# Kernel tuning notes

Hardware: AMD Instinct MI355X
Metric: run time of the kernel (lower is better)

The kernel has to match this reference:

```python
import jax, jax.numpy as jnp
import numpy as np

N_A, N_B = 50000, 20000   # authors, teams
E0, E1, E2 = 600000, 300000, 300000  # coauthor(A->A), writes(A->B), influences(B->A)
D = 128                   # in_feats = out_feats


def setup_inputs() -> dict:
    key = jax.random.key(0)
    ks = jax.random.split(key, 12)
    h_A = jax.random.normal(ks[0], (N_A, D), jnp.float32)
    h_B = jax.random.normal(ks[1], (N_B, D), jnp.float32)
    W0 = jax.random.normal(ks[2], (D, D), jnp.float32) * 0.05
    W1 = jax.random.normal(ks[3], (D, D), jnp.float32) * 0.05
    W2 = jax.random.normal(ks[4], (D, D), jnp.float32) * 0.05
    b0 = jnp.zeros((D,), jnp.float32)
    b1 = jnp.zeros((D,), jnp.float32)
    b2 = jnp.zeros((D,), jnp.float32)
    src0 = jax.random.randint(ks[5], (E0,), 0, N_A)
    dst0 = jax.random.randint(ks[6], (E0,), 0, N_A)
    src1 = jax.random.randint(ks[7], (E1,), 0, N_A)
    dst1 = jax.random.randint(ks[8], (E1,), 0, N_B)
    src2 = jax.random.randint(ks[9], (E2,), 0, N_B)
    dst2 = jax.random.randint(ks[10], (E2,), 0, N_A)
    return dict(h_A=h_A, h_B=h_B, W0=W0, b0=b0, W1=W1, b1=b1, W2=W2, b2=b2,
                src0=src0, dst0=dst0, src1=src1, dst1=dst1, src2=src2, dst2=dst2)


def _graph_conv(x_src, W, b, src, dst, n_dst):
    """DGL GraphConv, norm='both': out = D_dst^{-1/2} A D_src^{-1/2} (X W) + b."""
    n_src = x_src.shape[0]
    ones = jnp.ones(src.shape[0], x_src.dtype)
    deg_out = jnp.clip(jax.ops.segment_sum(ones, src, num_segments=n_src), 1.0)
    deg_in = jnp.clip(jax.ops.segment_sum(ones, dst, num_segments=n_dst), 1.0)
    m = (x_src @ W) * (deg_out ** -0.5)[:, None]          # [n_src, D]
    agg = jax.ops.segment_sum(m[src], dst, num_segments=n_dst)  # [n_dst, D]
    return agg * (deg_in ** -0.5)[:, None] + b


def reference(h_A, h_B, W0, b0, W1, b1, W2, b2, src0, dst0, src1, dst1, src2, dst2):
    # HeteroGraphConv(aggregate='sum'): sum per-relation GraphConv outputs per dst ntype.
    out_A = (_graph_conv(h_A, W0, b0, src0, dst0, N_A)
             + _graph_conv(h_B, W2, b2, src2, dst2, N_A))
    out_B = _graph_conv(h_A, W1, b1, src1, dst1, N_B)
    # every ntype present in h receives an output, so no passthrough branch fires
    return out_A, out_B
```

## Files before the change

kernel.cpp:

```cpp
#include <hip/hip_runtime.h>

#define NA 50000
#define NB 20000
#define NE0 600000
#define NE1 300000
#define NE2 300000
#define DD 128
#define SUB 32768
#define PER 18750


typedef short bf16x8 __attribute__((ext_vector_type(8)));
typedef float f32x4 __attribute__((ext_vector_type(4)));

__device__ __forceinline__ unsigned short f2bf(float f) {
    union { float f; unsigned int u; } v; v.f = f;
    unsigned int r = v.u + 0x7fffu + ((v.u >> 16) & 1u);
    return (unsigned short)(r >> 16);
}
__device__ __forceinline__ float lo2f(unsigned int u) {
    union { float f; unsigned int u; } v; v.u = u << 16;
    return v.f;
}
__device__ __forceinline__ float hi2f(unsigned int u) {
    union { float f; unsigned int u; } v; v.u = u & 0xffff0000u;
    return v.f;
}

__global__ __launch_bounds__(1024) void hist_kernel(
    const int* __restrict__ s0, const int* __restrict__ d0,
    const int* __restrict__ s1, const int* __restrict__ d1,
    const int* __restrict__ s2, const int* __restrict__ d2,
    unsigned int* __restrict__ Pd,
    unsigned char* __restrict__ rank0, unsigned char* __restrict__ rank1,
    unsigned char* __restrict__ rank2,
    const float* __restrict__ W0, const float* __restrict__ W1,
    const float* __restrict__ W2, unsigned short* __restrict__ Wt)
{
    __shared__ unsigned int h32[SUB / 2];
    const int cfg = blockIdx.z;
    if (cfg == 6) {
        int flat = blockIdx.y * 2 + blockIdx.x;
        if (flat >= 48) return;
        int i = flat * 1024 + threadIdx.x;
        int w = i >> 14, r = i & (DD * DD - 1);
        int c = r >> 7, k = r & (DD - 1);
        const float* W = (w == 0) ? W0 : ((w == 1) ? W1 : W2);
        Wt[i] = f2bf(W[k * DD + c]);
        return;
    }
    const int En[6] = {NE0, NE0, NE1, NE1, NE2, NE2};
    const int Kn[6] = {NA, NA, NA, NB, NB, NA};
    const int Gn[6] = {32, 32, 16, 16, 16, 16};
    const int Po[6] = {0, 1600000, 3200000, 4000000, 4320000, 4640000};
    int E = En[cfg], K = Kn[cfg], G = Gn[cfg];
    int sub = blockIdx.x, g = blockIdx.y;
    int nsub = (K + SUB - 1) / SUB;
    if (sub >= nsub || g >= G) return;
    const int* keys = cfg == 0 ? s0 : cfg == 1 ? d0 : cfg == 2 ? s1
                    : cfg == 3 ? d1 : cfg == 4 ? s2 : d2;
    unsigned char* rk = cfg == 1 ? rank0 : cfg == 3 ? rank1
                      : cfg == 5 ? rank2 : (unsigned char*)0;
    int lo = sub * SUB;
    int hi = min(K, lo + SUB);
    int cnt = hi - lo;
    for (int i = threadIdx.x; i < SUB / 2; i += 1024) h32[i] = 0;
    __syncthreads();
    int e1 = min(E, g * PER + PER);
    for (int e = g * PER + threadIdx.x; e < e1; e += 1024) {
        int k = keys[e];
        if (k >= lo && k < hi) {
            int kk = k - lo;
            unsigned sh = (kk & 1) << 4;
            unsigned old = atomicAdd(&h32[kk >> 1], 1u << sh);
            if (rk) rk[e] = (unsigned char)((old >> sh) & 0xffu);
        }
    }
    __syncthreads();
    unsigned int* outp = Pd + ((Po[cfg] + g * K + lo) >> 1);
    for (int i = threadIdx.x; i < cnt / 2; i += 1024) outp[i] = h32[i];
}

__global__ __launch_bounds__(256) void reduce2(
    const unsigned short* __restrict__ P16, int* __restrict__ ideg,
    float* __restrict__ rdeg, int* __restrict__ spart,
    unsigned char* __restrict__ cum8)
{
    __shared__ int lds[256];
    const int y = blockIdx.y;
    const int Ro[6] = {0, NA, 2 * NA, 3 * NA, 3 * NA + NB, 3 * NA + 2 * NB};
    const int Kr[6] = {NA, NA, NA, NB, NB, NA};
    const int Gr[6] = {32, 32, 16, 16, 16, 16};
    const int Po[6] = {0, 1600000, 3200000, 4000000, 4320000, 4640000};
    const int Co[6] = {0, 0, 0, 1600000, 0, 1920000};
    int K = Kr[y], G = Gr[y];
    int b = blockIdx.x, t = threadIdx.x;
    int nchunk = (K + 255) >> 8;
    if (b >= nchunk) return;
    int key = b * 256 + t;
    bool valid = key < K;
    bool din = (y == 1) || (y == 3) || (y == 5);
    const unsigned short* p = P16 + Po[y] + key;
    unsigned char* cb = cum8 + Co[y] + key;
    int run = 0;
    for (int g = 0; g < G; ++g) {
        if (din && valid) cb[g * K] = (unsigned char)run;
        run += valid ? p[g * K] : 0;
    }
    if (valid) {
        ideg[Ro[y] + key] = run;
        rdeg[Ro[y] + key] = rsqrtf(fmaxf((float)run, 1.f));
    }
    if (din) {
        int slot = (y - 1) >> 1;
        lds[t] = run; __syncthreads();
        for (int o = 128; o > 0; o >>= 1) {
            if (t < o) lds[t] += lds[t + o];
            __syncthreads();
        }
        if (t == 0) spart[slot * 256 + b] = lds[0];
    }
}

__global__ __launch_bounds__(256) void scan3(
    const int* __restrict__ ideg, const int* __restrict__ spart,
    int* __restrict__ rp)
{
    __shared__ int lds[256];
    const int y = blockIdx.y;
    const int off[3] = {NA, 3 * NA, 3 * NA + 2 * NB};
    const int nn[3]  = {NA, NB, NA};
    const int ro[3]  = {0, NA, NA + NB};
    int n = nn[y];
    int b = blockIdx.x, t = threadIdx.x;
    if (b * 1024 >= n) return;

    lds[t] = (t < 4 * b) ? spart[y * 256 + t] : 0;
    __syncthreads();
    for (int o = 128; o > 0; o >>= 1) {
        if (t < o) lds[t] += lds[t + o];
        __syncthreads();
    }
    int pv = lds[0];
    __syncthreads();

    const int* deg = ideg + off[y];
    int base = b * 1024 + t * 4;
    int v[4]; int tsum = 0;
    #pragma unroll
    for (int k = 0; k < 4; ++k) {
        v[k] = (base + k < n) ? deg[base + k] : 0;
        tsum += v[k];
    }
    lds[t] = tsum; __syncthreads();
    for (int o = 1; o < 256; o <<= 1) {
        int x = (t >= o) ? lds[t - o] : 0;
        __syncthreads();
        lds[t] += x;
        __syncthreads();
    }
    int run = lds[t] - tsum + pv;
    int* rowptr = rp + ro[y];
    #pragma unroll
    for (int k = 0; k < 4; ++k) {
        if (base + k < n) rowptr[base + k] = run;
        run += v[k];
    }
}

__global__ __launch_bounds__(512) void work_kernel(
    const int* __restrict__ s0, const int* __restrict__ d0,
    const int* __restrict__ s1, const int* __restrict__ d1,
    const int* __restrict__ s2, const int* __restrict__ d2,
    const unsigned char* __restrict__ cum8,
    const unsigned char* __restrict__ rank0, const unsigned char* __restrict__ rank1,
    const unsigned char* __restrict__ rank2,
    const int* __restrict__ rp,
    int* __restrict__ csr0, int* __restrict__ csr1, int* __restrict__ csr2,
    const float* __restrict__ hA, const float* __restrict__ hB,
    const unsigned short* __restrict__ Wt, const float* __restrict__ rdeg,
    unsigned short* __restrict__ mA0, unsigned short* __restrict__ mA1,
    unsigned short* __restrict__ mB2)
{
    int bx = blockIdx.x;
    int wid  = threadIdx.x >> 6;
    int lane = threadIdx.x & 63;
    int quad = lane >> 4;
    int l16  = lane & 15;
    if (bx < 391) {
        int base = bx * 128 + wid * 16;
        if (base >= NA) return;
        int arow = base + l16;
        if (arow >= NA) arow = NA - 1;
        bf16x8 a[4];
        #pragma unroll
        for (int kk = 0; kk < 4; ++kk) {
            const float4* p = (const float4*)(hA + (size_t)arow * DD + kk * 32 + quad * 8);
            float4 u = p[0], w = p[1];
            bf16x8 t;
            t[0] = (short)f2bf(u.x); t[1] = (short)f2bf(u.y);
            t[2] = (short)f2bf(u.z); t[3] = (short)f2bf(u.w);
            t[4] = (short)f2bf(w.x); t[5] = (short)f2bf(w.y);
            t[6] = (short)f2bf(w.z); t[7] = (short)f2bf(w.w);
            a[kk] = t;
        }
        float rs0[4], rs1[4]; int orow0 = base + quad * 4;
        #pragma unroll
        for (int r = 0; r < 4; ++r) {
            int orow = orow0 + r; int c = orow < NA ? orow : 0;
            rs0[r] = rdeg[c]; rs1[r] = rdeg[2 * NA + c];
        }
        #pragma unroll
        for (int ct = 0; ct < 8; ++ct) {
            f32x4 acc0 = {0.f, 0.f, 0.f, 0.f};
            f32x4 acc1 = {0.f, 0.f, 0.f, 0.f};
            const unsigned short* wp = Wt + (size_t)(ct * 16 + l16) * DD + quad * 8;
            #pragma unroll
            for (int kk = 0; kk < 4; ++kk) {
                bf16x8 b0 = *(const bf16x8*)(wp + kk * 32);
                bf16x8 b1 = *(const bf16x8*)(wp + 16384 + kk * 32);
                acc0 = __builtin_amdgcn_mfma_f32_16x16x32_bf16(a[kk], b0, acc0, 0, 0, 0);
                acc1 = __builtin_amdgcn_mfma_f32_16x16x32_bf16(a[kk], b1, acc1, 0, 0, 0);
            }
            #pragma unroll
            for (int r = 0; r < 4; ++r) {
                int orow = orow0 + r;
                if (orow < NA) {
                    mA0[(size_t)orow * DD + ct * 16 + l16] = f2bf(acc0[r] * rs0[r]);
                    mA1[(size_t)orow * DD + ct * 16 + l16] = f2bf(acc1[r] * rs1[r]);
                }
            }
        }
        return;
    }
    if (bx < 548) {
        int base = (bx - 391) * 128 + wid * 16;
        if (base >= NB) return;
        int arow = base + l16;
        if (arow >= NB) arow = NB - 1;
        bf16x8 a[4];
        #pragma unroll
        for (int kk = 0; kk < 4; ++kk) {
            const float4* p = (const float4*)(hB + (size_t)arow * DD + kk * 32 + quad * 8);
            float4 u = p[0], w = p[1];
            bf16x8 t;
            t[0] = (short)f2bf(u.x); t[1] = (short)f2bf(u.y);
            t[2] = (short)f2bf(u.z); t[3] = (short)f2bf(u.w);
            t[4] = (short)f2bf(w.x); t[5] = (short)f2bf(w.y);
            t[6] = (short)f2bf(w.z); t[7] = (short)f2bf(w.w);
            a[kk] = t;
        }
        float rs[4]; int orow0 = base + quad * 4;
        #pragma unroll
        for (int r = 0; r < 4; ++r) {
            int orow = orow0 + r;
            rs[r] = rdeg[3 * NA + NB + (orow < NB ? orow : 0)];
        }
        #pragma unroll
        for (int ct = 0; ct < 8; ++ct) {
            f32x4 acc = {0.f, 0.f, 0.f, 0.f};
            const unsigned short* wp = Wt + 32768 + (size_t)(ct * 16 + l16) * DD + quad * 8;
            #pragma unroll
            for (int kk = 0; kk < 4; ++kk) {
                bf16x8 b = *(const bf16x8*)(wp + kk * 32);
                acc = __builtin_amdgcn_mfma_f32_16x16x32_bf16(a[kk], b, acc, 0, 0, 0);
            }
            #pragma unroll
            for (int r = 0; r < 4; ++r) {
                int orow = orow0 + r;
                if (orow < NB)
                    mB2[(size_t)orow * DD + ct * 16 + l16] = f2bf(acc[r] * rs[r]);
            }
        }
        return;
    }
    int pb = bx - 548;
    int z = (pb < 586) ? 0 : (pb < 879) ? 1 : 2;
    const int zb[3] = {0, 586, 879};
    const int En[3] = {NE0, NE1, NE2};
    const int Kn[3] = {NA, NB, NA};
    const int Co[3] = {0, 1600000, 1920000};
    const int ro[3] = {0, NA, NA + NB};
    int E = En[z], K = Kn[z];
    const int* src = z == 0 ? s0 : z == 1 ? s1 : s2;
    const int* dst = z == 0 ? d0 : z == 1 ? d1 : d2;
    const unsigned char* rk = z == 0 ? rank0 : z == 1 ? rank1 : rank2;
    int* csr = z == 0 ? csr0 : z == 1 ? csr1 : csr2;
    int e0 = (pb - zb[z]) * 1024 + threadIdx.x;
    int e1 = e0 + 512;
    bool v0 = e0 < E, v1 = e1 < E;
    int ce0 = v0 ? e0 : 0, ce1 = v1 ? e1 : 0;
    int d_0 = dst[ce0];
    int d_1 = dst[ce1];
    int r_0 = rk[ce0];
    int r_1 = rk[ce1];
    int s_0 = src[ce0];
    int s_1 = src[ce1];
    int g0 = ce0 / PER;
    int g1 = ce1 / PER;
    int p0 = rp[ro[z] + d_0] + (int)cum8[Co[z] + g0 * K + d_0] + r_0;
    int p1 = rp[ro[z] + d_1] + (int)cum8[Co[z] + g1 * K + d_1] + r_1;
    if (v0) csr[p0] = s_0;
    if (v1) csr[p1] = s_1;
}

__device__ __forceinline__ void acc8(float* o, uint4 u) {
    o[0] += lo2f(u.x); o[1] += hi2f(u.x);
    o[2] += lo2f(u.y); o[3] += hi2f(u.y);
    o[4] += lo2f(u.z); o[5] += hi2f(u.z);
    o[6] += lo2f(u.w); o[7] += hi2f(u.w);
}
__device__ __forceinline__ void gather_rel4(
    const char* __restrict__ Mb, const int* __restrict__ csr,
    int st, int n, int lane, int q, unsigned laneoff, float* o)
{
    for (int ch = 0; ch < n; ch += 64) {
        int m = n - ch; if (m > 64) m = 64;
        int idx = csr[st + ch + (lane < m ? lane : m - 1)];
        int j = 0;
        for (; j + 8 <= m; j += 8) {
            int sA = __shfl(idx, j + q);
            int sB = __shfl(idx, j + 4 + q);
            uint4 uA = *(const uint4*)(Mb + (((unsigned)sA << 8) + laneoff));
            uint4 uB = *(const uint4*)(Mb + (((unsigned)sB << 8) + laneoff));
            acc8(o, uA); acc8(o, uB);
        }
        if (j + 4 <= m) {
            int s = __shfl(idx, j + q);
            uint4 u = *(const uint4*)(Mb + (((unsigned)s << 8) + laneoff));
            acc8(o, u);
            j += 4;
        }
        if (j < m) {
            int jj = j + q;
            float w = jj < m ? 1.f : 0.f;
            int s = __shfl(idx, jj < m ? jj : m - 1);
            uint4 u = *(const uint4*)(Mb + (((unsigned)s << 8) + laneoff));
            o[0] = fmaf(w, lo2f(u.x), o[0]); o[1] = fmaf(w, hi2f(u.x), o[1]);
            o[2] = fmaf(w, lo2f(u.y), o[2]); o[3] = fmaf(w, hi2f(u.y), o[3]);
            o[4] = fmaf(w, lo2f(u.z), o[4]); o[5] = fmaf(w, hi2f(u.z), o[5]);
            o[6] = fmaf(w, lo2f(u.w), o[6]); o[7] = fmaf(w, hi2f(u.w), o[7]);
        }
    }
}

__global__ __launch_bounds__(256) void gather_all(
    const unsigned short* __restrict__ mA0, const unsigned short* __restrict__ mA1,
    const unsigned short* __restrict__ mB2,
    const int* __restrict__ csr0, const int* __restrict__ csr1,
    const int* __restrict__ csr2,
    const int* __restrict__ rp, const int* __restrict__ ideg,
    const float* __restrict__ rdeg,
    const float* __restrict__ b0, const float* __restrict__ b1,
    const float* __restrict__ b2,
    float* __restrict__ out)
{
    int wid = threadIdx.x >> 6, lane = threadIdx.x & 63;
    int q = lane >> 4, l16 = lane & 15;
    unsigned laneoff = (unsigned)l16 * 16u;
    float v[8];
    #pragma unroll
    for (int i = 0; i < 8; ++i) v[i] = 0.f;
    float* op;
    const float *bia, *bib;

    if (blockIdx.x < 12500) {
        int d = blockIdx.x * 4 + wid;
        float c[8];
        #pragma unroll
        for (int i = 0; i < 8; ++i) c[i] = 0.f;
        gather_rel4((const char*)mA0, csr0, rp[d], ideg[NA + d], lane, q, laneoff, v);
        gather_rel4((const char*)mB2, csr2, rp[NA + NB + d], ideg[3 * NA + 2 * NB + d],
                    lane, q, laneoff, c);
        float r0 = rdeg[NA + d], r2 = rdeg[3 * NA + 2 * NB + d];
        #pragma unroll
        for (int i = 0; i < 8; ++i) v[i] = v[i] * r0 + c[i] * r2;
        op = out + (size_t)d * DD;
        bia = b0; bib = b2;
    } else {
        int d = (blockIdx.x - 12500) * 4 + wid;
        gather_rel4((const char*)mA1, csr1, rp[NA + d], ideg[3 * NA + d],
                    lane, q, laneoff, v);
        float r1 = rdeg[3 * NA + d];
        #pragma unroll
        for (int i = 0; i < 8; ++i) v[i] *= r1;
        op = out + (size_t)(NA + d) * DD;
        bia = b1; bib = 0;
    }

    #pragma unroll
    for (int i = 0; i < 8; ++i) {
        v[i] += __shfl_down(v[i], 32);
        v[i] += __shfl_down(v[i], 16);
    }
    if (lane < 16) {
        int col = l16 * 8;
        float4 ba0 = *(const float4*)(bia + col);
        float4 ba1 = *(const float4*)(bia + col + 4);
        if (bib) {
            float4 bb0 = *(const float4*)(bib + col);
            float4 bb1 = *(const float4*)(bib + col + 4);
            ba0.x += bb0.x; ba0.y += bb0.y; ba0.z += bb0.z; ba0.w += bb0.w;
            ba1.x += bb1.x; ba1.y += bb1.y; ba1.z += bb1.z; ba1.w += bb1.w;
        }
        float4 o0 = {v[0] + ba0.x, v[1] + ba0.y, v[2] + ba0.z, v[3] + ba0.w};
        float4 o1 = {v[4] + ba1.x, v[5] + ba1.y, v[6] + ba1.z, v[7] + ba1.w};
        *(float4*)(op + col) = o0;
        *(float4*)(op + col + 4) = o1;
    }
}

extern "C" void kernel_launch(void* const* d_in, const int* in_sizes, int n_in,
                              void* d_out, int out_size, void* d_ws, size_t ws_size,
                              hipStream_t stream) {
    const float* hA = (const float*)d_in[0];
    const float* hB = (const float*)d_in[1];
    const float* W0 = (const float*)d_in[2];
    const float* b0 = (const float*)d_in[3];
    const float* W1 = (const float*)d_in[4];
    const float* b1 = (const float*)d_in[5];
    const float* W2 = (const float*)d_in[6];
    const float* b2 = (const float*)d_in[7];
    const int* s0 = (const int*)d_in[8];
    const int* d0 = (const int*)d_in[9];
    const int* s1 = (const int*)d_in[10];
    const int* d1 = (const int*)d_in[11];
    const int* s2 = (const int*)d_in[12];
    const int* d2 = (const int*)d_in[13];
    float* out = (float*)d_out;
    char* ws = (char*)d_ws;

    unsigned short* mA0 = (unsigned short*)(ws + 0);
    unsigned short* mA1 = (unsigned short*)(ws + 12800000);
    unsigned short* mB2 = (unsigned short*)(ws + 25600000);
    unsigned short* P16 = (unsigned short*)(ws + 0);
    unsigned int*   Pd  = (unsigned int*)(ws + 0);
    unsigned short* Wt  = (unsigned short*)(ws + 30720000);
    float* rdeg         = (float*)(ws + 30818304);
    int*   ideg         = (int*)  (ws + 31778304);
    int*   rp           = (int*)  (ws + 32738304);
    int*   spart        = (int*)  (ws + 33218304);
    unsigned char* cum8 = (unsigned char*)(ws + 33221376);
    unsigned char* rank0= (unsigned char*)(ws + 35941376);
    unsigned char* rank1= (unsigned char*)(ws + 36541376);
    unsigned char* rank2= (unsigned char*)(ws + 36841376);
    int*   csr0         = (int*)  (ws + 37141376);
    int*   csr1         = (int*)  (ws + 39541376);
    int*   csr2         = (int*)  (ws + 40741376);

    hist_kernel<<<dim3(2, 32, 7), 1024, 0, stream>>>(s0, d0, s1, d1, s2, d2,
        Pd, rank0, rank1, rank2, W0, W1, W2, Wt);
    reduce2<<<dim3(196, 6), 256, 0, stream>>>(P16, ideg, rdeg, spart, cum8);
    scan3<<<dim3(49, 3), 256, 0, stream>>>(ideg, spart, rp);
    work_kernel<<<548 + 1172, 512, 0, stream>>>(s0, d0, s1, d1, s2, d2,
        cum8, rank0, rank1, rank2, rp, csr0, csr1, csr2,
        hA, hB, Wt, rdeg, mA0, mA1, mB2);
    gather_all<<<12500 + 5000, 256, 0, stream>>>(mA0, mA1, mB2,
        csr0, csr1, csr2, rp, ideg, rdeg, b0, b1, b2, out);
}
```

Measured before the change: 237.3 us.

## Precompute CSR scatter positions in scan and store CSR indices as u16

The scan kernel now also writes a per-(group, destination) absolute position table, rowptr plus cum8, into the output buffer, which serves as scratch. The scatter kernel then does one lookup instead of two, and each thread handles four edges instead of two, launched on half as many blocks. CSR source indices are stored as 16-bit values, which fit because node counts are at most 50000, to cut index bytes in the scatter and gather passes. In exchange the scan kernel does a long serial per-thread loop writing about 2.7M ints with few blocks. That extra scan work could offset the savings.

```diff
diff --git a/kernel.cpp b/kernel.cpp
--- a/kernel.cpp
+++ b/kernel.cpp
@@ -124,13 +124,16 @@
 
 __global__ __launch_bounds__(256) void scan3(
     const int* __restrict__ ideg, const int* __restrict__ spart,
-    int* __restrict__ rp)
+    int* __restrict__ rp, const unsigned char* __restrict__ cum8,
+    int* __restrict__ pos32)
 {
     __shared__ int lds[256];
     const int y = blockIdx.y;
     const int off[3] = {NA, 3 * NA, 3 * NA + 2 * NB};
     const int nn[3]  = {NA, NB, NA};
     const int ro[3]  = {0, NA, NA + NB};
+    const int Gy[3]  = {32, 16, 16};
+    const int Coy[3] = {0, 1600000, 1920000};
     int n = nn[y];
     int b = blockIdx.x, t = threadIdx.x;
     if (b * 1024 >= n) return;
@@ -161,10 +164,24 @@
     }
     int run = lds[t] - tsum + pv;
     int* rowptr = rp + ro[y];
+    int rv[4];
     #pragma unroll
     for (int k = 0; k < 4; ++k) {
+        rv[k] = run;
         if (base + k < n) rowptr[base + k] = run;
         run += v[k];
+    }
+    int G = Gy[y];
+    const int Co_ = Coy[y];
+    for (int g = 0; g < G; ++g) {
+        #pragma unroll
+        for (int k = 0; k < 4; ++k) {
+            int key = base + k;
+            if (key < n) {
+                int c = Co_ + g * n + key;
+                pos32[c] = rv[k] + (int)cum8[c];
+            }
+        }
     }
 }
 
@@ -172,11 +189,11 @@
     const int* __restrict__ s0, const int* __restrict__ d0,
     const int* __restrict__ s1, const int* __restrict__ d1,
     const int* __restrict__ s2, const int* __restrict__ d2,
-    const unsigned char* __restrict__ cum8,
     const unsigned char* __restrict__ rank0, const unsigned char* __restrict__ rank1,
     const unsigned char* __restrict__ rank2,
-    const int* __restrict__ rp,
-    int* __restrict__ csr0, int* __restrict__ csr1, int* __restrict__ csr2,
+    const int* __restrict__ pos32,
+    unsigned short* __restrict__ csr0, unsigned short* __restrict__ csr1,
+    unsigned short* __restrict__ csr2,
     const float* __restrict__ hA, const float* __restrict__ hB,
     const unsigned short* __restrict__ Wt, const float* __restrict__ rdeg,
     unsigned short* __restrict__ mA0, unsigned short* __restrict__ mA1,
@@ -275,33 +292,40 @@
         return;
     }
     int pb = bx - 548;
-    int z = (pb < 586) ? 0 : (pb < 879) ? 1 : 2;
-    const int zb[3] = {0, 586, 879};
+    int z = (pb < 293) ? 0 : (pb < 440) ? 1 : 2;
+    const int zb[3] = {0, 293, 440};
     const int En[3] = {NE0, NE1, NE2};
     const int Kn[3] = {NA, NB, NA};
     const int Co[3] = {0, 1600000, 1920000};
-    const int ro[3] = {0, NA, NA + NB};
     int E = En[z], K = Kn[z];
     const int* src = z == 0 ? s0 : z == 1 ? s1 : s2;
     const int* dst = z == 0 ? d0 : z == 1 ? d1 : d2;
     const unsigned char* rk = z == 0 ? rank0 : z == 1 ? rank1 : rank2;
-    int* csr = z == 0 ? csr0 : z == 1 ? csr1 : csr2;
-    int e0 = (pb - zb[z]) * 1024 + threadIdx.x;
-    int e1 = e0 + 512;
-    bool v0 = e0 < E, v1 = e1 < E;
-    int ce0 = v0 ? e0 : 0, ce1 = v1 ? e1 : 0;
-    int d_0 = dst[ce0];
-    int d_1 = dst[ce1];
-    int r_0 = rk[ce0];
-    int r_1 = rk[ce1];
-    int s_0 = src[ce0];
-    int s_1 = src[ce1];
-    int g0 = ce0 / PER;
-    int g1 = ce1 / PER;
-    int p0 = rp[ro[z] + d_0] + (int)cum8[Co[z] + g0 * K + d_0] + r_0;
-    int p1 = rp[ro[z] + d_1] + (int)cum8[Co[z] + g1 * K + d_1] + r_1;
-    if (v0) csr[p0] = s_0;
-    if (v1) csr[p1] = s_1;
+    unsigned short* csr = z == 0 ? csr0 : z == 1 ? csr1 : csr2;
+    int ebase = (pb - zb[z]) * 2048 + threadIdx.x;
+    int ce[4]; bool vv[4];
+    #pragma unroll
+    for (int j = 0; j < 4; ++j) {
+        int e = ebase + j * 512;
+        vv[j] = e < E;
+        ce[j] = vv[j] ? e : 0;
+    }
+    int dd_[4], rr[4], ss[4];
+    #pragma unroll
+    for (int j = 0; j < 4; ++j) dd_[j] = dst[ce[j]];
+    #pragma unroll
+    for (int j = 0; j < 4; ++j) rr[j] = rk[ce[j]];
+    #pragma unroll
+    for (int j = 0; j < 4; ++j) ss[j] = src[ce[j]];
+    int pp[4];
+    #pragma unroll
+    for (int j = 0; j < 4; ++j) {
+        int g = ce[j] / PER;
+        pp[j] = pos32[Co[z] + g * K + dd_[j]] + rr[j];
+    }
+    #pragma unroll
+    for (int j = 0; j < 4; ++j)
+        if (vv[j]) csr[pp[j]] = (unsigned short)ss[j];
 }
 
 __device__ __forceinline__ void acc8(float* o, uint4 u) {
@@ -311,7 +335,7 @@
     o[6] += lo2f(u.w); o[7] += hi2f(u.w);
 }
 __device__ __forceinline__ void gather_rel4(
-    const char* __restrict__ Mb, const int* __restrict__ csr,
+    const char* __restrict__ Mb, const unsigned short* __restrict__ csr,
     int st, int n, int lane, int q, unsigned laneoff, float* o)
 {
     for (int ch = 0; ch < n; ch += 64) {
@@ -347,8 +371,8 @@
 __global__ __launch_bounds__(256) void gather_all(
     const unsigned short* __restrict__ mA0, const unsigned short* __restrict__ mA1,
     const unsigned short* __restrict__ mB2,
-    const int* __restrict__ csr0, const int* __restrict__ csr1,
-    const int* __restrict__ csr2,
+    const unsigned short* __restrict__ csr0, const unsigned short* __restrict__ csr1,
+    const unsigned short* __restrict__ csr2,
     const int* __restrict__ rp, const int* __restrict__ ideg,
     const float* __restrict__ rdeg,
     const float* __restrict__ b0, const float* __restrict__ b1,
@@ -444,16 +468,17 @@
     unsigned char* rank0= (unsigned char*)(ws + 35941376);
     unsigned char* rank1= (unsigned char*)(ws + 36541376);
     unsigned char* rank2= (unsigned char*)(ws + 36841376);
-    int*   csr0         = (int*)  (ws + 37141376);
-    int*   csr1         = (int*)  (ws + 39541376);
-    int*   csr2         = (int*)  (ws + 40741376);
+    unsigned short* csr0= (unsigned short*)(ws + 37141376);
+    unsigned short* csr1= (unsigned short*)(ws + 38341376);
+    unsigned short* csr2= (unsigned short*)(ws + 38941376);
+    int*            pos32 = (int*)d_out;
 
     hist_kernel<<<dim3(2, 32, 7), 1024, 0, stream>>>(s0, d0, s1, d1, s2, d2,
         Pd, rank0, rank1, rank2, W0, W1, W2, Wt);
     reduce2<<<dim3(196, 6), 256, 0, stream>>>(P16, ideg, rdeg, spart, cum8);
-    scan3<<<dim3(49, 3), 256, 0, stream>>>(ideg, spart, rp);
-    work_kernel<<<548 + 1172, 512, 0, stream>>>(s0, d0, s1, d1, s2, d2,
-        cum8, rank0, rank1, rank2, rp, csr0, csr1, csr2,
+    scan3<<<dim3(49, 3), 256, 0, stream>>>(ideg, spart, rp, cum8, pos32);
+    work_kernel<<<548 + 587, 512, 0, stream>>>(s0, d0, s1, d1, s2, d2,
+        rank0, rank1, rank2, pos32, csr0, csr1, csr2,
         hA, hB, Wt, rdeg, mA0, mA1, mB2);
     gather_all<<<12500 + 5000, 256, 0, stream>>>(mA0, mA1, mB2,
         csr0, csr1, csr2, rp, ideg, rdeg, b0, b1, b2, out);
```

Measured after the change: 264.3 us. 1.11x slower.
